# Kernel optimization log

Hardware: AMD Instinct MI355X
Metric: run time of the kernel (lower is better)

Reference implementation:

```python
import jax, jax.numpy as jnp
import numpy as np

B, F, H, D, TE, CE = 16384, 1024, 64, 256, 4, 4

def setup_inputs() -> dict:
    key = jax.random.key(0)
    ks = iter(jax.random.split(key, 40))
    s = 0.02
    mk = lambda shape: jax.random.normal(next(ks), shape, jnp.float32) * s
    inp = {
        'x_A': jax.random.normal(next(ks), (B, F), jnp.float32),
        'x_S': jax.random.normal(next(ks), (B, F), jnp.float32),
        'x_B': jax.random.normal(next(ks), (B, F), jnp.float32),
        # stacked per-expert weights for the three expert groups (A, Shared, B)
        'W1A': mk((TE, F, H)), 'b1A': mk((TE, H)), 'W2A': mk((TE, H, D)), 'b2A': mk((TE, D)),
        'W1S': mk((CE, F, H)), 'b1S': mk((CE, H)), 'W2S': mk((CE, H, D)), 'b2S': mk((CE, D)),
        'W1B': mk((TE, F, H)), 'b1B': mk((TE, H)), 'W2B': mk((TE, H, D)), 'b2B': mk((TE, D)),
        # gate weights
        'WgA': mk((F, TE + CE)), 'bgA': mk((TE + CE,)),
        'WgB': mk((F, TE + CE)), 'bgB': mk((TE + CE,)),
        'WgS': mk((F, 2 * TE + CE)), 'bgS': mk((2 * TE + CE,)),
    }
    return inp

def _expert_group(x, W1, b1, W2, b2):
    # x: [B,F], W1: [E,F,H] -> [B,E,H]; W2: [E,H,D] -> [B,E,D]
    h = jax.nn.relu(jnp.einsum('bf,efh->beh', x, W1) + b1)  # dropout p=0 -> identity
    return jax.nn.relu(jnp.einsum('beh,ehd->bed', h, W2) + b2)

def reference(x_A, x_S, x_B,
              W1A, b1A, W2A, b2A,
              W1S, b1S, W2S, b2S,
              W1B, b1B, W2B, b2B,
              WgA, bgA, WgB, bgB, WgS, bgS):
    EA = _expert_group(x_A, W1A, b1A, W2A, b2A)  # [B,TE,D]
    ES = _expert_group(x_S, W1S, b1S, W2S, b2S)  # [B,CE,D]
    EB = _expert_group(x_B, W1B, b1B, W2B, b2B)  # [B,TE,D]
    gA = jax.nn.softmax(x_A @ WgA + bgA, axis=1)  # [B,TE+CE]
    gS = jax.nn.softmax(x_S @ WgS + bgS, axis=1)  # [B,2TE+CE]
    gB = jax.nn.softmax(x_B @ WgB + bgB, axis=1)  # [B,TE+CE]
    outA = jnp.einsum('bed,be->bd', jnp.concatenate([EA, ES], axis=1), gA)
    outS = jnp.einsum('bed,be->bd', jnp.concatenate([EA, ES, EB], axis=1), gS)
    outB = jnp.einsum('bed,be->bd', jnp.concatenate([EB, ES], axis=1), gB)
    return (outA, outS, outB)
```

## Files before the change

kernel.cpp:

```cpp
#include <hip/hip_runtime.h>


#define BB 16384
#define FF 1024

typedef _Float16 f16;
typedef __fp16 h16x2 __attribute__((ext_vector_type(2)));
typedef _Float16 f16x8 __attribute__((ext_vector_type(8)));
typedef float f32x4 __attribute__((ext_vector_type(4)));

__device__ __forceinline__ void load_lds16(const void* g, void* l) {
    __builtin_amdgcn_global_load_lds(
        (const __attribute__((address_space(1))) unsigned int*)g,
        (__attribute__((address_space(3))) unsigned int*)l, 16, 0, 0);
}

__device__ __forceinline__ f16x8 pack8(float4 lo, float4 hi) {
    union { f16x8 v; h16x2 p[4]; } u;
    u.p[0] = __builtin_amdgcn_cvt_pkrtz(lo.x, lo.y);
    u.p[1] = __builtin_amdgcn_cvt_pkrtz(lo.z, lo.w);
    u.p[2] = __builtin_amdgcn_cvt_pkrtz(hi.x, hi.y);
    u.p[3] = __builtin_amdgcn_cvt_pkrtz(hi.z, hi.w);
    return u.v;
}

__device__ __forceinline__ int expert_gi(int o, int k) {
    if (o == 0) return (k < 4) ? 0 : 1;
    if (o == 1) return k >> 2;
    return (k < 4) ? 2 : 1;
}

__global__ __launch_bounds__(256) void pack_kernel(
    const float* __restrict__ W1A, const float* __restrict__ W1S, const float* __restrict__ W1B,
    const float* __restrict__ W2A, const float* __restrict__ W2S, const float* __restrict__ W2B,
    const float* __restrict__ WgA, const float* __restrict__ WgS, const float* __restrict__ WgB,
    f16* __restrict__ W1F, f16* __restrict__ W2F, f16* __restrict__ Gp2)
{
    int idx = blockIdx.x * 256 + threadIdx.x;
    if (idx < 786432) {
        int g = idx / 262144, r = idx % 262144;
        int nt = r >> 14, r2 = r & 16383;
        int kt = r2 >> 9, s = r2 & 511;
        int lane = s >> 3, j = s & 7;
        int c = nt * 16 + (lane & 15);
        int k = kt * 32 + (lane >> 4) * 8 + j;
        const float* W1 = (g == 0) ? W1A : ((g == 1) ? W1S : W1B);
        W1F[idx] = (f16)W1[((c >> 6) << 16) + k * 64 + (c & 63)];
    } else if (idx < 983040) {
        int t = idx - 786432;
        int g = t / 65536, r = t % 65536;
        int e = r >> 14, r2 = r & 16383;
        int nt = r2 >> 10, r3 = r2 & 1023;
        int kt = r3 >> 9, s = r3 & 511;
        int lane = s >> 3, j = s & 7;
        int d = nt * 16 + (lane & 15);
        int hh = kt * 32 + (lane >> 4) * 8 + j;
        const float* W2 = (g == 0) ? W2A : ((g == 1) ? W2S : W2B);
        W2F[t] = (f16)W2[e * 16384 + hh * 256 + d];
    } else {
        int t = idx - 983040;
        int g = t / 16384, rem = t % 16384;
        int c = rem >> 10, k = rem & 1023;
        int ng = (g == 1) ? 12 : 8;
        const float* Wg = (g == 0) ? WgA : ((g == 1) ? WgS : WgB);
        Gp2[t] = (c < ng) ? (f16)Wg[k * ng + c] : (f16)0.0f;
    }
}

__global__ __launch_bounds__(512, 4) void l1_kernel(
    const float* __restrict__ xA, const float* __restrict__ xS, const float* __restrict__ xB,
    const float* __restrict__ b1A, const float* __restrict__ b1S, const float* __restrict__ b1B,
    const float* __restrict__ bgA, const float* __restrict__ bgS, const float* __restrict__ bgB,
    const f16* __restrict__ W1F,
    const f16* __restrict__ Gp2,
    f16* __restrict__ hbuf,
    float* __restrict__ gates)
{
    const int g = blockIdx.y;
    const float* x  = (g == 0) ? xA  : ((g == 1) ? xS  : xB);
    const float* b1 = (g == 0) ? b1A : ((g == 1) ? b1S : b1B);
    const float* bg = (g == 0) ? bgA : ((g == 1) ? bgS : bgB);
    const int ng = (g == 1) ? 12 : 8;
    float* gout = gates + ((g == 0) ? (size_t)0
                         : (g == 1) ? (size_t)BB * 8
                                    : (size_t)BB * 8 + (size_t)BB * 12);

    const int row0 = blockIdx.x * 128;

    __shared__ __align__(16) f16 Ash[2][128 * 32];

    const int tid  = threadIdx.x;
    const int lane = tid & 63;
    const int wave = tid >> 6;
    const int wm = (wave >> 2) * 64;
    const int wn = (wave & 3) * 64;
    const int lrow = lane & 15;
    const int quad = lane >> 4;
    const bool my_gate = ((wave & 3) == 0);

    const f16* Wbase = W1F + (size_t)g * 262144;
    const f16* Ggrp  = Gp2 + ((size_t)g * 16 + lrow) * 1024 + quad * 8;

    const int am = tid >> 2;
    const int ac = tid & 3;
    const float* xld = x + (size_t)(row0 + am) * FF + ac * 8;
    const int aoff = am * 32 + ac * 8;

    f32x4 acc[4][4] = {};
    f32x4 gacc[4] = {};

    {
        float4 lo = *(const float4*)(xld);
        float4 hi = *(const float4*)(xld + 4);
        *(f16x8*)(&Ash[0][aoff]) = pack8(lo, hi);
    }
    __syncthreads();

    for (int kt = 0; kt < 32; ++kt) {
        const int cur = kt & 1, nxt = cur ^ 1;
        float4 lo, hi;
        if (kt < 31) {
            lo = *(const float4*)(xld + (kt + 1) * 32);
            hi = *(const float4*)(xld + (kt + 1) * 32 + 4);
        }
        f16x8 gb;
        if (my_gate) gb = *(const f16x8*)(Ggrp + kt * 32);

        f16x8 bf[4];
#pragma unroll
        for (int j = 0; j < 4; ++j) {
            int nt = (wn >> 4) + j;
            bf[j] = *(const f16x8*)(Wbase + ((size_t)nt * 32 + kt) * 512 + lane * 8);
        }
#pragma unroll
        for (int i = 0; i < 4; ++i) {
            f16x8 a = *(const f16x8*)(&Ash[cur][(wm + i * 16 + lrow) * 32 + quad * 8]);
#pragma unroll
            for (int j = 0; j < 4; ++j)
                acc[i][j] = __builtin_amdgcn_mfma_f32_16x16x32_f16(a, bf[j], acc[i][j], 0, 0, 0);
            if (my_gate)
                gacc[i] = __builtin_amdgcn_mfma_f32_16x16x32_f16(a, gb, gacc[i], 0, 0, 0);
        }
        if (kt < 31)
            *(f16x8*)(&Ash[nxt][aoff]) = pack8(lo, hi);
        __syncthreads();
    }

#pragma unroll
    for (int j = 0; j < 4; ++j) {
        int c = wn + j * 16 + lrow;
        float bias = b1[c];
#pragma unroll
        for (int i = 0; i < 4; ++i) {
#pragma unroll
            for (int r = 0; r < 4; ++r) {
                int row = row0 + wm + i * 16 + quad * 4 + r;
                float v = fmaxf(acc[i][j][r] + bias, 0.0f);
                hbuf[((size_t)g * BB + row) * 256 + c] = (f16)v;
            }
        }
    }

    if (my_gate) {
        int c = lrow;
        bool valid = (c < ng);
        float bias = valid ? bg[c] : 0.0f;
#pragma unroll
        for (int i = 0; i < 4; ++i) {
#pragma unroll
            for (int r = 0; r < 4; ++r) {
                int row = row0 + wm + i * 16 + quad * 4 + r;
                float logit = valid ? (gacc[i][r] + bias) : -1e30f;
                float mx = logit;
#pragma unroll
                for (int m = 1; m < 16; m <<= 1)
                    mx = fmaxf(mx, __shfl_xor(mx, m, 16));
                float ev = valid ? __expf(logit - mx) : 0.0f;
                float sum = ev;
#pragma unroll
                for (int m = 1; m < 16; m <<= 1)
                    sum += __shfl_xor(sum, m, 16);
                if (valid) gout[(size_t)row * ng + c] = ev / sum;
            }
        }
    }
}

__global__ __launch_bounds__(512, 4) void l2_kernel(
    const f16* __restrict__ hbuf,
    const f16* __restrict__ W2F,
    const float* __restrict__ b2A, const float* __restrict__ b2S, const float* __restrict__ b2B,
    const float* __restrict__ gates,
    float* __restrict__ out)
{
    const int o = blockIdx.y;
    const int row0 = blockIdx.x * 128;
    const int tid = threadIdx.x;
    const int lane = tid & 63;
    const int wave = tid >> 6;
    const int wm = (wave >> 1) * 32;
    const int wn = (wave & 1) * 128;
    const int lrow = lane & 15;
    const int quad = lane >> 4;

    const int ng = (o == 1) ? 12 : 8;
    const float* gp = gates + ((o == 0) ? (size_t)0
                             : (o == 1) ? (size_t)BB * 8
                                        : (size_t)BB * 8 + (size_t)BB * 12);

    __shared__ __align__(16) f16 Ash[2][128 * 64];
    __shared__ float gsh[128 * 12];

    for (int idx = tid; idx < 128 * ng; idx += 512)
        gsh[idx] = gp[(size_t)(row0 + idx / ng) * ng + (idx % ng)];

    {
        int gi = expert_gi(o, 0);
        const f16* hs = hbuf + ((size_t)gi * BB + row0) * 256;
#pragma unroll
        for (int r = 0; r < 2; ++r) {
            int s = r * 512 + tid;
            int m = s >> 3, slot = s & 7;
            int chunk = slot ^ (m & 7);
            load_lds16(hs + (size_t)m * 256 + chunk * 8, &Ash[0][s * 8]);
        }
    }

    f32x4 oacc[2][8] = {};

    for (int k = 0; k < ng; ++k) {
        const int cur = k & 1, nxt = cur ^ 1;
        __syncthreads();

        if (k + 1 < ng) {
            int gi2 = expert_gi(o, k + 1);
            int e2 = (k + 1) & 3;
            const f16* hs = hbuf + ((size_t)gi2 * BB + row0) * 256 + e2 * 64;
#pragma unroll
            for (int r = 0; r < 2; ++r) {
                int s = r * 512 + tid;
                int m = s >> 3, slot = s & 7;
                int chunk = slot ^ (m & 7);
                load_lds16(hs + (size_t)m * 256 + chunk * 8, &Ash[nxt][s * 8]);
            }
        }

        const int e = k & 3;
        const int gi = expert_gi(o, k);
        const float* b2 = (gi == 0) ? b2A : ((gi == 1) ? b2S : b2B);
        const f16* wb = W2F + (size_t)(gi * 4 + e) * 16384;

        f16x8 af[2][2];
#pragma unroll
        for (int i = 0; i < 2; ++i) {
#pragma unroll
            for (int kk = 0; kk < 2; ++kk) {
                int m = wm + i * 16 + lrow;
                int slot = (kk * 4 + quad) ^ (m & 7);
                af[i][kk] = *(const f16x8*)(&Ash[cur][m * 64 + slot * 8]);
            }
        }
#pragma unroll
        for (int j = 0; j < 8; ++j) {
            int nt = (wn >> 4) + j;
            f16x8 bf0 = *(const f16x8*)(wb + ((size_t)nt * 2 + 0) * 512 + lane * 8);
            f16x8 bf1 = *(const f16x8*)(wb + ((size_t)nt * 2 + 1) * 512 + lane * 8);
            int d = wn + j * 16 + lrow;
            float bias = b2[e * 256 + d];
#pragma unroll
            for (int i = 0; i < 2; ++i) {
                f32x4 t = {};
                t = __builtin_amdgcn_mfma_f32_16x16x32_f16(af[i][0], bf0, t, 0, 0, 0);
                t = __builtin_amdgcn_mfma_f32_16x16x32_f16(af[i][1], bf1, t, 0, 0, 0);
#pragma unroll
                for (int r = 0; r < 4; ++r) {
                    int rl = wm + i * 16 + quad * 4 + r;
                    float v = fmaxf(t[r] + bias, 0.0f);
                    oacc[i][j][r] += gsh[rl * ng + k] * v;
                }
            }
        }
    }

#pragma unroll
    for (int j = 0; j < 8; ++j) {
        int d = wn + j * 16 + lrow;
#pragma unroll
        for (int i = 0; i < 2; ++i) {
#pragma unroll
            for (int r = 0; r < 4; ++r) {
                int rl = wm + i * 16 + quad * 4 + r;
                out[((size_t)o * BB + row0 + rl) * 256 + d] = oacc[i][j][r];
            }
        }
    }
}

extern "C" void kernel_launch(void* const* d_in, const int* in_sizes, int n_in,
                              void* d_out, int out_size, void* d_ws, size_t ws_size,
                              hipStream_t stream)
{
    (void)in_sizes; (void)n_in; (void)out_size; (void)ws_size;

    const float* xA  = (const float*)d_in[0];
    const float* xS  = (const float*)d_in[1];
    const float* xB  = (const float*)d_in[2];
    const float* W1A = (const float*)d_in[3];
    const float* b1A = (const float*)d_in[4];
    const float* W2A = (const float*)d_in[5];
    const float* b2A = (const float*)d_in[6];
    const float* W1S = (const float*)d_in[7];
    const float* b1S = (const float*)d_in[8];
    const float* W2S = (const float*)d_in[9];
    const float* b2S = (const float*)d_in[10];
    const float* W1B = (const float*)d_in[11];
    const float* b1B = (const float*)d_in[12];
    const float* W2B = (const float*)d_in[13];
    const float* b2B = (const float*)d_in[14];
    const float* WgA = (const float*)d_in[15];
    const float* bgA = (const float*)d_in[16];
    const float* WgB = (const float*)d_in[17];
    const float* bgB = (const float*)d_in[18];
    const float* WgS = (const float*)d_in[19];
    const float* bgS = (const float*)d_in[20];

    char* ws = (char*)d_ws;
    f16*   W1F  = (f16*)(ws);
    f16*   W2F  = (f16*)(ws + 0x180000);
    f16*   Gp2  = (f16*)(ws + 0x1E0000);
    f16*   hbuf = (f16*)(ws + 0x200000);
    float* gate = (float*)(ws + 0x200000 + 0x1800000);

    pack_kernel<<<4032, 256, 0, stream>>>(W1A, W1S, W1B, W2A, W2S, W2B,
                                          WgA, WgS, WgB, W1F, W2F, Gp2);
    l1_kernel<<<dim3(128, 3), 512, 0, stream>>>(
        xA, xS, xB, b1A, b1S, b1B, bgA, bgS, bgB,
        W1F, Gp2, hbuf, gate);
    l2_kernel<<<dim3(128, 3), 512, 0, stream>>>(
        hbuf, W2F, b2A, b2S, b2B, gate, (float*)d_out);
}
```

Baseline: 342.4 us.

## Shrink row tiles to 32 rows with 256-thread blocks for more CTAs

Both GEMM kernels now process 32 rows per block with 4 waves, each wave covering 64 output columns, and launch 512x3 blocks instead of 128x3. The goal is to fill all compute units on the GPU, since only 384 blocks were launched before. The L1 kernel takes K steps of 64 with an XOR-swizzled LDS tile. The L2 kernel replaces async global-to-LDS loads with register staging and caches gate weights in registers. The cost is that W1 and W2 weight fragments are re-read from global memory or L2 by four times as many blocks, so each block reuses them less.

```diff
diff --git a/kernel.cpp b/kernel.cpp
--- a/kernel.cpp
+++ b/kernel.cpp
@@ -8,20 +8,16 @@
 typedef __fp16 h16x2 __attribute__((ext_vector_type(2)));
 typedef _Float16 f16x8 __attribute__((ext_vector_type(8)));
 typedef float f32x4 __attribute__((ext_vector_type(4)));
-
-__device__ __forceinline__ void load_lds16(const void* g, void* l) {
-    __builtin_amdgcn_global_load_lds(
-        (const __attribute__((address_space(1))) unsigned int*)g,
-        (__attribute__((address_space(3))) unsigned int*)l, 16, 0, 0);
-}
+typedef unsigned int u32;
+typedef u32 u32x4 __attribute__((ext_vector_type(4)));
 
 __device__ __forceinline__ f16x8 pack8(float4 lo, float4 hi) {
-    union { f16x8 v; h16x2 p[4]; } u;
-    u.p[0] = __builtin_amdgcn_cvt_pkrtz(lo.x, lo.y);
-    u.p[1] = __builtin_amdgcn_cvt_pkrtz(lo.z, lo.w);
-    u.p[2] = __builtin_amdgcn_cvt_pkrtz(hi.x, hi.y);
-    u.p[3] = __builtin_amdgcn_cvt_pkrtz(hi.z, hi.w);
-    return u.v;
+    u32 w0 = __builtin_bit_cast(u32, __builtin_amdgcn_cvt_pkrtz(lo.x, lo.y));
+    u32 w1 = __builtin_bit_cast(u32, __builtin_amdgcn_cvt_pkrtz(lo.z, lo.w));
+    u32 w2 = __builtin_bit_cast(u32, __builtin_amdgcn_cvt_pkrtz(hi.x, hi.y));
+    u32 w3 = __builtin_bit_cast(u32, __builtin_amdgcn_cvt_pkrtz(hi.z, hi.w));
+    u32x4 u = {w0, w1, w2, w3};
+    return __builtin_bit_cast(f16x8, u);
 }
 
 __device__ __forceinline__ int expert_gi(int o, int k) {
@@ -67,7 +63,7 @@
     }
 }
 
-__global__ __launch_bounds__(512, 4) void l1_kernel(
+__global__ __launch_bounds__(256, 4) void l1_kernel(
     const float* __restrict__ xA, const float* __restrict__ xS, const float* __restrict__ xB,
     const float* __restrict__ b1A, const float* __restrict__ b1S, const float* __restrict__ b1B,
     const float* __restrict__ bgA, const float* __restrict__ bgS, const float* __restrict__ bgB,
@@ -85,64 +81,73 @@
                          : (g == 1) ? (size_t)BB * 8
                                     : (size_t)BB * 8 + (size_t)BB * 12);
 
-    const int row0 = blockIdx.x * 128;
-
-    __shared__ __align__(16) f16 Ash[2][128 * 32];
+    const int row0 = blockIdx.x * 32;
+
+    __shared__ __align__(16) f16 Ash[2][32 * 64];
 
     const int tid  = threadIdx.x;
     const int lane = tid & 63;
     const int wave = tid >> 6;
-    const int wm = (wave >> 2) * 64;
-    const int wn = (wave & 3) * 64;
+    const int wn   = wave * 64;
     const int lrow = lane & 15;
     const int quad = lane >> 4;
-    const bool my_gate = ((wave & 3) == 0);
+    const bool my_gate = (wave == 0);
 
     const f16* Wbase = W1F + (size_t)g * 262144;
     const f16* Ggrp  = Gp2 + ((size_t)g * 16 + lrow) * 1024 + quad * 8;
 
-    const int am = tid >> 2;
-    const int ac = tid & 3;
+    const int am = tid >> 3;
+    const int ac = tid & 7;
     const float* xld = x + (size_t)(row0 + am) * FF + ac * 8;
-    const int aoff = am * 32 + ac * 8;
-
-    f32x4 acc[4][4] = {};
-    f32x4 gacc[4] = {};
-
-    {
-        float4 lo = *(const float4*)(xld);
-        float4 hi = *(const float4*)(xld + 4);
-        *(f16x8*)(&Ash[0][aoff]) = pack8(lo, hi);
-    }
-    __syncthreads();
-
-    for (int kt = 0; kt < 32; ++kt) {
-        const int cur = kt & 1, nxt = cur ^ 1;
-        float4 lo, hi;
-        if (kt < 31) {
-            lo = *(const float4*)(xld + (kt + 1) * 32);
-            hi = *(const float4*)(xld + (kt + 1) * 32 + 4);
-        }
-        f16x8 gb;
-        if (my_gate) gb = *(const f16x8*)(Ggrp + kt * 32);
-
-        f16x8 bf[4];
-#pragma unroll
-        for (int j = 0; j < 4; ++j) {
-            int nt = (wn >> 4) + j;
-            bf[j] = *(const f16x8*)(Wbase + ((size_t)nt * 32 + kt) * 512 + lane * 8);
-        }
-#pragma unroll
-        for (int i = 0; i < 4; ++i) {
-            f16x8 a = *(const f16x8*)(&Ash[cur][(wm + i * 16 + lrow) * 32 + quad * 8]);
-#pragma unroll
-            for (int j = 0; j < 4; ++j)
-                acc[i][j] = __builtin_amdgcn_mfma_f32_16x16x32_f16(a, bf[j], acc[i][j], 0, 0, 0);
-            if (my_gate)
-                gacc[i] = __builtin_amdgcn_mfma_f32_16x16x32_f16(a, gb, gacc[i], 0, 0, 0);
-        }
-        if (kt < 31)
-            *(f16x8*)(&Ash[nxt][aoff]) = pack8(lo, hi);
+    const int aoff = am * 64 + (ac ^ (am & 7)) * 8;
+
+    f32x4 acc[2][4] = {};
+    f32x4 gacc[2] = {};
+
+    float4 lo = *(const float4*)(xld);
+    float4 hi = *(const float4*)(xld + 4);
+
+    for (int kt = 0; kt < 16; ++kt) {
+        const int cur = kt & 1;
+        *(f16x8*)(&Ash[cur][aoff]) = pack8(lo, hi);
+        __syncthreads();
+
+        f16x8 bf[8];
+#pragma unroll
+        for (int jk = 0; jk < 8; ++jk) {
+            int nt = (wn >> 4) + (jk >> 1);
+            int kk = jk & 1;
+            bf[jk] = *(const f16x8*)(Wbase + ((size_t)nt * 32 + kt * 2 + kk) * 512 + lane * 8);
+        }
+        f16x8 gb0, gb1;
+        if (my_gate) {
+            gb0 = *(const f16x8*)(Ggrp + kt * 64);
+            gb1 = *(const f16x8*)(Ggrp + kt * 64 + 32);
+        }
+        if (kt < 15) {
+            lo = *(const float4*)(xld + (kt + 1) * 64);
+            hi = *(const float4*)(xld + (kt + 1) * 64 + 4);
+        }
+
+        f16x8 af[2][2];
+#pragma unroll
+        for (int i = 0; i < 2; ++i)
+#pragma unroll
+            for (int kk = 0; kk < 2; ++kk)
+                af[i][kk] = *(const f16x8*)(&Ash[cur][(i * 16 + lrow) * 64 +
+                                                      (((kk * 4 + quad) ^ (lrow & 7)) * 8)]);
+#pragma unroll
+        for (int kk = 0; kk < 2; ++kk)
+#pragma unroll
+            for (int i = 0; i < 2; ++i) {
+#pragma unroll
+                for (int j = 0; j < 4; ++j)
+                    acc[i][j] = __builtin_amdgcn_mfma_f32_16x16x32_f16(
+                        af[i][kk], bf[j * 2 + kk], acc[i][j], 0, 0, 0);
+                if (my_gate)
+                    gacc[i] = __builtin_amdgcn_mfma_f32_16x16x32_f16(
+                        af[i][kk], (kk == 0) ? gb0 : gb1, gacc[i], 0, 0, 0);
+            }
         __syncthreads();
     }
 
@@ -151,10 +156,10 @@
         int c = wn + j * 16 + lrow;
         float bias = b1[c];
 #pragma unroll
-        for (int i = 0; i < 4; ++i) {
+        for (int i = 0; i < 2; ++i) {
 #pragma unroll
             for (int r = 0; r < 4; ++r) {
-                int row = row0 + wm + i * 16 + quad * 4 + r;
+                int row = row0 + i * 16 + quad * 4 + r;
                 float v = fmaxf(acc[i][j][r] + bias, 0.0f);
                 hbuf[((size_t)g * BB + row) * 256 + c] = (f16)v;
             }
@@ -166,10 +171,10 @@
         bool valid = (c < ng);
         float bias = valid ? bg[c] : 0.0f;
 #pragma unroll
-        for (int i = 0; i < 4; ++i) {
+        for (int i = 0; i < 2; ++i) {
 #pragma unroll
             for (int r = 0; r < 4; ++r) {
-                int row = row0 + wm + i * 16 + quad * 4 + r;
+                int row = row0 + i * 16 + quad * 4 + r;
                 float logit = valid ? (gacc[i][r] + bias) : -1e30f;
                 float mx = logit;
 #pragma unroll
@@ -186,7 +191,7 @@
     }
 }
 
-__global__ __launch_bounds__(512, 4) void l2_kernel(
+__global__ __launch_bounds__(256, 4) void l2_kernel(
     const f16* __restrict__ hbuf,
     const f16* __restrict__ W2F,
     const float* __restrict__ b2A, const float* __restrict__ b2S, const float* __restrict__ b2B,
@@ -194,12 +199,11 @@
     float* __restrict__ out)
 {
     const int o = blockIdx.y;
-    const int row0 = blockIdx.x * 128;
+    const int row0 = blockIdx.x * 32;
     const int tid = threadIdx.x;
     const int lane = tid & 63;
     const int wave = tid >> 6;
-    const int wm = (wave >> 1) * 32;
-    const int wn = (wave & 1) * 128;
+    const int wn = wave * 64;
     const int lrow = lane & 15;
     const int quad = lane >> 4;
 
@@ -208,88 +212,90 @@
                              : (o == 1) ? (size_t)BB * 8
                                         : (size_t)BB * 8 + (size_t)BB * 12);
 
-    __shared__ __align__(16) f16 Ash[2][128 * 64];
-    __shared__ float gsh[128 * 12];
-
-    for (int idx = tid; idx < 128 * ng; idx += 512)
+    __shared__ __align__(16) f16 Ash[2][32 * 64];
+    __shared__ float gsh[32 * 12];
+
+    for (int idx = tid; idx < 32 * ng; idx += 256)
         gsh[idx] = gp[(size_t)(row0 + idx / ng) * ng + (idx % ng)];
 
+    const int am = tid >> 3;
+    const int ac = tid & 7;
+    const int aoff = am * 64 + (ac ^ (am & 7)) * 8;
+
+    u32x4 hreg;
     {
-        int gi = expert_gi(o, 0);
-        const f16* hs = hbuf + ((size_t)gi * BB + row0) * 256;
-#pragma unroll
-        for (int r = 0; r < 2; ++r) {
-            int s = r * 512 + tid;
-            int m = s >> 3, slot = s & 7;
-            int chunk = slot ^ (m & 7);
-            load_lds16(hs + (size_t)m * 256 + chunk * 8, &Ash[0][s * 8]);
-        }
-    }
-
-    f32x4 oacc[2][8] = {};
+        int gi0 = expert_gi(o, 0);
+        const f16* hs = hbuf + ((size_t)gi0 * BB + row0) * 256;
+        hreg = *(const u32x4*)(hs + (size_t)am * 256 + ac * 8);
+    }
+
+    f32x4 oacc[2][4] = {};
 
     for (int k = 0; k < ng; ++k) {
-        const int cur = k & 1, nxt = cur ^ 1;
+        const int cur = k & 1;
+        *(u32x4*)(&Ash[cur][aoff]) = hreg;
         __syncthreads();
 
+        const int e = k & 3;
+        const int gi = expert_gi(o, k);
+        const float* b2 = (gi == 0) ? b2A : ((gi == 1) ? b2S : b2B);
+        const f16* wb = W2F + (size_t)(gi * 4 + e) * 16384;
+
+        f16x8 bf[8];
+#pragma unroll
+        for (int jk = 0; jk < 8; ++jk) {
+            int nt = (wn >> 4) + (jk >> 1);
+            int kk = jk & 1;
+            bf[jk] = *(const f16x8*)(wb + ((size_t)nt * 2 + kk) * 512 + lane * 8);
+        }
         if (k + 1 < ng) {
             int gi2 = expert_gi(o, k + 1);
             int e2 = (k + 1) & 3;
             const f16* hs = hbuf + ((size_t)gi2 * BB + row0) * 256 + e2 * 64;
-#pragma unroll
-            for (int r = 0; r < 2; ++r) {
-                int s = r * 512 + tid;
-                int m = s >> 3, slot = s & 7;
-                int chunk = slot ^ (m & 7);
-                load_lds16(hs + (size_t)m * 256 + chunk * 8, &Ash[nxt][s * 8]);
-            }
-        }
-
-        const int e = k & 3;
-        const int gi = expert_gi(o, k);
-        const float* b2 = (gi == 0) ? b2A : ((gi == 1) ? b2S : b2B);
-        const f16* wb = W2F + (size_t)(gi * 4 + e) * 16384;
+            hreg = *(const u32x4*)(hs + (size_t)am * 256 + ac * 8);
+        }
+
+        float gw[2][4];
+#pragma unroll
+        for (int i = 0; i < 2; ++i)
+#pragma unroll
+            for (int r = 0; r < 4; ++r)
+                gw[i][r] = gsh[(i * 16 + quad * 4 + r) * ng + k];
 
         f16x8 af[2][2];
 #pragma unroll
-        for (int i = 0; i < 2; ++i) {
-#pragma unroll
-            for (int kk = 0; kk < 2; ++kk) {
-                int m = wm + i * 16 + lrow;
-                int slot = (kk * 4 + quad) ^ (m & 7);
-                af[i][kk] = *(const f16x8*)(&Ash[cur][m * 64 + slot * 8]);
-            }
-        }
-#pragma unroll
-        for (int j = 0; j < 8; ++j) {
-            int nt = (wn >> 4) + j;
-            f16x8 bf0 = *(const f16x8*)(wb + ((size_t)nt * 2 + 0) * 512 + lane * 8);
-            f16x8 bf1 = *(const f16x8*)(wb + ((size_t)nt * 2 + 1) * 512 + lane * 8);
+        for (int i = 0; i < 2; ++i)
+#pragma unroll
+            for (int kk = 0; kk < 2; ++kk)
+                af[i][kk] = *(const f16x8*)(&Ash[cur][(i * 16 + lrow) * 64 +
+                                                      (((kk * 4 + quad) ^ (lrow & 7)) * 8)]);
+#pragma unroll
+        for (int j = 0; j < 4; ++j) {
             int d = wn + j * 16 + lrow;
             float bias = b2[e * 256 + d];
 #pragma unroll
             for (int i = 0; i < 2; ++i) {
                 f32x4 t = {};
-                t = __builtin_amdgcn_mfma_f32_16x16x32_f16(af[i][0], bf0, t, 0, 0, 0);
-                t = __builtin_amdgcn_mfma_f32_16x16x32_f16(af[i][1], bf1, t, 0, 0, 0);
+                t = __builtin_amdgcn_mfma_f32_16x16x32_f16(af[i][0], bf[j * 2 + 0], t, 0, 0, 0);
+                t = __builtin_amdgcn_mfma_f32_16x16x32_f16(af[i][1], bf[j * 2 + 1], t, 0, 0, 0);
 #pragma unroll
                 for (int r = 0; r < 4; ++r) {
-                    int rl = wm + i * 16 + quad * 4 + r;
                     float v = fmaxf(t[r] + bias, 0.0f);
-                    oacc[i][j][r] += gsh[rl * ng + k] * v;
+                    oacc[i][j][r] += gw[i][r] * v;
                 }
             }
         }
-    }
-
-#pragma unroll
-    for (int j = 0; j < 8; ++j) {
+        __syncthreads();
+    }
+
+#pragma unroll
+    for (int j = 0; j < 4; ++j) {
         int d = wn + j * 16 + lrow;
 #pragma unroll
         for (int i = 0; i < 2; ++i) {
 #pragma unroll
             for (int r = 0; r < 4; ++r) {
-                int rl = wm + i * 16 + quad * 4 + r;
+                int rl = i * 16 + quad * 4 + r;
                 out[((size_t)o * BB + row0 + rl) * 256 + d] = oacc[i][j][r];
             }
         }
@@ -333,9 +339,9 @@
 
     pack_kernel<<<4032, 256, 0, stream>>>(W1A, W1S, W1B, W2A, W2S, W2B,
                                           WgA, WgS, WgB, W1F, W2F, Gp2);
-    l1_kernel<<<dim3(128, 3), 512, 0, stream>>>(
+    l1_kernel<<<dim3(512, 3), 256, 0, stream>>>(
         xA, xS, xB, b1A, b1S, b1B, bgA, bgS, bgB,
         W1F, Gp2, hbuf, gate);
-    l2_kernel<<<dim3(128, 3), 512, 0, stream>>>(
+    l2_kernel<<<dim3(512, 3), 256, 0, stream>>>(
         hbuf, W2F, b2A, b2S, b2B, gate, (float*)d_out);
 }
```

Measured after the change: 398.2 us. 16.3% more time.
